# Kernel tuning notes

Measured on AMD Instinct MI355X. Metric: run time of the kernel, lower is better.

The kernel has to match this reference:

```python
import jax, jax.numpy as jnp
import numpy as np

B, S, D, H = 2, 2048, 1024, 16
DK = D // H


def setup_inputs() -> dict:
    key = jax.random.key(0)
    ks = jax.random.split(key, 8)
    q = jax.random.normal(ks[0], (B, S, D), dtype=jnp.float32)
    k = jax.random.normal(ks[1], (B, S, D), dtype=jnp.float32)
    v = jax.random.normal(ks[2], (B, S, D), dtype=jnp.float32)
    mask = jax.random.randint(ks[3], (B, 1, S, S), 0, 2, dtype=jnp.int32)
    sc = 1.0 / np.sqrt(D)
    Wq = jax.random.normal(ks[4], (D, D), dtype=jnp.float32) * sc
    Wk = jax.random.normal(ks[5], (D, D), dtype=jnp.float32) * sc
    Wv = jax.random.normal(ks[6], (D, D), dtype=jnp.float32) * sc
    Wo = jax.random.normal(ks[7], (D, D), dtype=jnp.float32) * sc
    return {"q": q, "k": k, "v": v, "mask": mask, "Wq": Wq, "Wk": Wk, "Wv": Wv, "Wo": Wo}


def reference(q, k, v, mask, Wq, Wk, Wv, Wo):
    # Linear projections (torch Linear: x @ W.T; bias=False). Weights here stored
    # as [D, D] applied as x @ W (equivalent parameterization).
    query = q @ Wq  # [B,S,D]
    key = k @ Wk
    value = v @ Wv
    # split heads -> [B,H,S,DK]
    query = query.reshape(B, S, H, DK).transpose(0, 2, 1, 3)
    key = key.reshape(B, S, H, DK).transpose(0, 2, 1, 3)
    value = value.reshape(B, S, H, DK).transpose(0, 2, 1, 3)
    scores = jnp.einsum('bhqd,bhkd->bhqk', query, key) / jnp.sqrt(jnp.float32(DK))
    scores = jnp.where(mask == 0, jnp.float32(-1e9), scores)
    probs = jax.nn.softmax(scores, axis=-1)  # dropout p=0.0 -> identity
    x = jnp.einsum('bhqk,bhkd->bhqd', probs, value)
    x = x.transpose(0, 2, 1, 3).reshape(B, S, D)
    return x @ Wo
```

## Files before the change

kernel.cpp:

```cpp
#include <hip/hip_runtime.h>
#include <hip/hip_bf16.h>
#include <math.h>

#define B_ 2
#define S_ 2048
#define D_ 1024
#define H_ 16
#define DK_ 64
#define SW_ (S_ / 64)

typedef unsigned short u16;
typedef unsigned int u32;
typedef unsigned long long u64;
typedef __attribute__((ext_vector_type(8))) short short8;
typedef __attribute__((ext_vector_type(4))) float float4_;
typedef __attribute__((ext_vector_type(4))) unsigned int uint4_;

static __device__ inline u16 f_to_bf16(float f) {
    union { float f; u32 i; } x; x.f = f;
    u32 r = x.i + 0x7fff + ((x.i >> 16) & 1);
    return (u16)(r >> 16);
}

static __device__ __forceinline__ u32 cvtpk(float a, float b) {
    u32 r;
    asm("v_cvt_pk_bf16_f32 %0, %1, %2" : "=v"(r) : "v"(a), "v"(b));
    return r;
}

static __device__ __forceinline__ float fast_exp2(float x) {
#if __has_builtin(__builtin_amdgcn_exp2f)
    return __builtin_amdgcn_exp2f(x);
#else
    return exp2f(x);
#endif
}

static __device__ inline void gl_lds16(const u16* g, u16* l) {
    __builtin_amdgcn_global_load_lds((const __attribute__((address_space(1))) void*)g,
                                     (__attribute__((address_space(3))) void*)l, 16, 0, 0);
}

__global__ __launch_bounds__(256) void prep(const float* __restrict__ q,
                                            const float* __restrict__ k,
                                            const float* __restrict__ v,
                                            const int* __restrict__ mask,
                                            const float* __restrict__ W0,
                                            const float* __restrict__ W1,
                                            const float* __restrict__ W2,
                                            const float* __restrict__ W3,
                                            u16* __restrict__ qb, u16* __restrict__ kb,
                                            u16* __restrict__ vb,
                                            u16* __restrict__ T0, u16* __restrict__ T1,
                                            u16* __restrict__ T2, u16* __restrict__ T3,
                                            u64* __restrict__ mpk) {
    __shared__ float tile[32][33];
    int gx = blockIdx.x, tid = threadIdx.x;
    if (gx < 6144) {
        int z = gx >> 11;
        int bx = gx & 2047;
        const float* s = (z == 0) ? q : ((z == 1) ? k : v);
        u16* d = (z == 0) ? qb : ((z == 1) ? kb : vb);
        int i = (bx * 256 + tid) * 8;
        #pragma unroll
        for (int j = 0; j < 8; ++j) d[i + j] = f_to_bf16(s[i + j]);
    } else if (gx < 10240) {
        int g2 = gx - 6144;
        int z = g2 >> 10;
        int rem = g2 & 1023;
        const float* W = (z == 0) ? W0 : ((z == 1) ? W1 : ((z == 2) ? W2 : W3));
        u16* Wt = (z == 0) ? T0 : ((z == 1) ? T1 : ((z == 2) ? T2 : T3));
        int k0 = (rem >> 5) * 32, n0 = (rem & 31) * 32;
        int tx = tid & 31, ty = tid >> 5;
        #pragma unroll
        for (int i2 = 0; i2 < 4; ++i2) {
            int row = ty + i2 * 8;
            tile[row][tx] = W[(size_t)(k0 + row) * D_ + n0 + tx];
        }
        __syncthreads();
        #pragma unroll
        for (int i2 = 0; i2 < 4; ++i2) {
            int row = ty + i2 * 8;
            Wt[(size_t)(n0 + row) * D_ + k0 + tx] = f_to_bf16(tile[tx][row]);
        }
    } else {
        int g3 = gx - 10240;
        int wv = (g3 * 256 + tid) >> 6;
        int lane = tid & 63;
        #pragma unroll
        for (int i2 = 0; i2 < 8; ++i2) {
            int wd = wv * 8 + i2;
            u64 bits = __ballot(mask[(size_t)wd * 64 + lane] != 0);
            if (lane == 0) mpk[wd] = bits;
        }
    }
}

static __device__ __forceinline__ void gemm128_body(u16* lds,
                                                    const u16* __restrict__ A,
                                                    const u16* __restrict__ Bt,
                                                    int K, float4_ (&acc)[4][4]) {
    u16* ldsA = lds;
    u16* ldsB = lds + 4096;
    int tm = blockIdx.x, tn = blockIdx.y;
    int t = threadIdx.x, l = t & 63;
    int w = t >> 6, wr = w >> 1, wc = w & 1;
    int colL = l & 15, grp = l >> 4;
    int sw4 = (grp ^ ((colL >> 1) & 3)) << 3;
    int f0 = t, f1 = t + 256;
    int row0 = f0 >> 2, kc0 = (((f0 & 3) ^ ((f0 >> 3) & 3)) << 3);
    int row1 = f1 >> 2, kc1 = (((f1 & 3) ^ ((f1 >> 3) & 3)) << 3);
    const u16* gA0 = A  + (size_t)(tm * 128 + row0) * K + kc0;
    const u16* gA1 = A  + (size_t)(tm * 128 + row1) * K + kc1;
    const u16* gB0 = Bt + (size_t)(tn * 128 + row0) * K + kc0;
    const u16* gB1 = Bt + (size_t)(tn * 128 + row1) * K + kc1;

    #pragma unroll
    for (int mi = 0; mi < 4; ++mi)
        #pragma unroll
        for (int ni = 0; ni < 4; ++ni)
            acc[mi][ni] = (float4_){0.f, 0.f, 0.f, 0.f};

    for (int k0 = 0; k0 < K; k0 += 32) {
        __syncthreads();
        gl_lds16(gA0 + k0, ldsA + f0 * 8);
        gl_lds16(gA1 + k0, ldsA + f1 * 8);
        gl_lds16(gB0 + k0, ldsB + f0 * 8);
        gl_lds16(gB1 + k0, ldsB + f1 * 8);
        __syncthreads();
        short8 a[4], b[4];
        #pragma unroll
        for (int mi = 0; mi < 4; ++mi)
            a[mi] = *(const short8*)&ldsA[(wr * 64 + mi * 16 + colL) * 32 + sw4];
        #pragma unroll
        for (int ni = 0; ni < 4; ++ni)
            b[ni] = *(const short8*)&ldsB[(wc * 64 + ni * 16 + colL) * 32 + sw4];
        #pragma unroll
        for (int mi = 0; mi < 4; ++mi)
            #pragma unroll
            for (int ni = 0; ni < 4; ++ni)
                acc[mi][ni] = __builtin_amdgcn_mfma_f32_16x16x32_bf16(a[mi], b[ni], acc[mi][ni], 0, 0, 0);
    }
}

__global__ __launch_bounds__(256, 3) void gemm_qkv(const u16* __restrict__ qb,
                                                   const u16* __restrict__ kb,
                                                   const u16* __restrict__ vb,
                                                   const u16* __restrict__ Wqt,
                                                   const u16* __restrict__ Wkt,
                                                   const u16* __restrict__ Wvt,
                                                   u16* __restrict__ Qp,
                                                   u16* __restrict__ Kp,
                                                   u16* __restrict__ Vt) {
    __shared__ u16 lds[8192];
    int z = blockIdx.z;
    const u16* A  = (z == 0) ? qb  : ((z == 1) ? kb  : vb);
    const u16* Bt = (z == 0) ? Wqt : ((z == 1) ? Wkt : Wvt);
    float4_ acc[4][4];
    gemm128_body(lds, A, Bt, D_, acc);

    int tm = blockIdx.x, tn = blockIdx.y;
    int t = threadIdx.x, l = t & 63;
    int w = t >> 6, wr = w >> 1, wc = w & 1;
    int colL = l & 15, grp = l >> 4;

    if (z < 2) {
        u16* Y = (z == 0) ? Qp : Kp;
        float sc = (z == 0) ? (0.125f * 1.44269504f) : 1.0f;
        #pragma unroll
        for (int mi = 0; mi < 4; ++mi)
            #pragma unroll
            for (int ni = 0; ni < 4; ++ni)
                #pragma unroll
                for (int r = 0; r < 4; ++r)
                    Y[(size_t)(tm * 128 + wr * 64 + mi * 16 + grp * 4 + r) * D_
                      + tn * 128 + wc * 64 + ni * 16 + colL] = f_to_bf16(acc[mi][ni][r] * sc);
    } else {
        int tok_base = tm * 128 + wr * 64;
        int bb = tok_base >> 11;
        int s_hi = tok_base & (S_ - 1);
        #pragma unroll
        for (int mi = 0; mi < 4; ++mi)
            #pragma unroll
            for (int ni = 0; ni < 4; ++ni) {
                int n  = tn * 128 + wc * 64 + ni * 16 + colL;
                int hh = n >> 6, dk = n & 63;
                u16* vp = Vt + ((size_t)(bb * H_ + hh) * DK_ + dk) * S_ + s_hi;
                #pragma unroll
                for (int r = 0; r < 4; ++r) {
                    int m = mi * 16 + grp * 4 + r;
                    int mp_ = ((m >> 5) & 1) * 32 + ((m >> 2) & 3) * 8 + ((m >> 4) & 1) * 4 + (m & 3);
                    vp[mp_] = f_to_bf16(acc[mi][ni][r]);
                }
            }
    }
}

__global__ __launch_bounds__(256, 3) void gemm_out(const u16* __restrict__ Xa,
                                                   const u16* __restrict__ Wot,
                                                   float* __restrict__ out) {
    __shared__ u16 lds[8192];
    float4_ acc[4][4];
    gemm128_body(lds, Xa, Wot, D_, acc);

    int tm = blockIdx.x, tn = blockIdx.y;
    int t = threadIdx.x, l = t & 63;
    int w = t >> 6, wr = w >> 1, wc = w & 1;
    int colL = l & 15, grp = l >> 4;
    #pragma unroll
    for (int mi = 0; mi < 4; ++mi)
        #pragma unroll
        for (int ni = 0; ni < 4; ++ni)
            #pragma unroll
            for (int r = 0; r < 4; ++r)
                out[(size_t)(tm * 128 + wr * 64 + mi * 16 + grp * 4 + r) * D_
                    + tn * 128 + wc * 64 + ni * 16 + colL] = acc[mi][ni][r];
}

__global__ __launch_bounds__(256, 2) void attn128(const u16* __restrict__ Qp,
                                                  const u16* __restrict__ Kp,
                                                  const u16* __restrict__ Vt,
                                                  const u64* __restrict__ mp,
                                                  u16* __restrict__ Xa) {
    __shared__ u16 ldsK[128 * 64];
    __shared__ u16 ldsV[2 * 64 * 64];

    int bid = blockIdx.x;
    int qt = bid & 15, h = (bid >> 4) & 15, b = bid >> 8;
    int t = threadIdx.x, l = t & 63, w = t >> 6;
    int colL = l & 15, grp = l >> 4;

    const u16* qbA = Qp + (size_t)(b * S_ + qt * 128 + w * 32 + colL) * D_ + h * DK_;
    const u16* qbB = qbA + (size_t)16 * D_;
    short8 qfA0 = *(const short8*)(qbA + grp * 8);
    short8 qfA1 = *(const short8*)(qbA + 32 + grp * 8);
    short8 qfB0 = *(const short8*)(qbB + grp * 8);
    short8 qfB1 = *(const short8*)(qbB + 32 + grp * 8);

    const u16* gK[4];
    const u16* gV[4];
    #pragma unroll
    for (int i = 0; i < 4; ++i) {
        int f = t + 256 * i;
        int krow = f >> 3, kch = (((f & 7) ^ (krow & 7)) << 3);
        gK[i] = Kp + (size_t)(b * S_ + krow) * D_ + h * DK_ + kch;
        int hreg = f >> 9, fp = f & 511;
        int vrow = fp >> 3, vch = (((fp & 7) ^ (vrow & 7)) << 3);
        gV[i] = Vt + ((size_t)(b * H_ + h) * DK_ + vrow) * S_ + hreg * 64 + vch;
    }

    int sw8 = (grp ^ (colL & 7)) << 3;

    short8 onesb;
    #pragma unroll
    for (int j = 0; j < 8; ++j) onesb[j] = (short)0x3F80;

    float4_ laccA = (float4_){0.f, 0.f, 0.f, 0.f};
    float4_ laccB = (float4_){0.f, 0.f, 0.f, 0.f};
    float4_ oA[4], oB[4];
    #pragma unroll
    for (int nt = 0; nt < 4; ++nt) {
        oA[nt] = (float4_){0.f, 0.f, 0.f, 0.f};
        oB[nt] = (float4_){0.f, 0.f, 0.f, 0.f};
    }

    const u64* mrA = mp + (size_t)(b * S_ + qt * 128 + w * 32 + colL) * SW_;
    const u64* mrB = mrA + (size_t)16 * SW_;

    for (int kt = 0; kt < S_; kt += 128) {
        u64 mwA0 = mrA[(kt >> 6)];
        u64 mwA1 = mrA[(kt >> 6) + 1];
        u64 mwB0 = mrB[(kt >> 6)];
        u64 mwB1 = mrB[(kt >> 6) + 1];

        __syncthreads();
        #pragma unroll
        for (int i = 0; i < 4; ++i) {
            int f = t + 256 * i;
            gl_lds16(gK[i] + (size_t)kt * D_, ldsK + f * 8);
            gl_lds16(gV[i] + kt,              ldsV + f * 8);
        }
        __syncthreads();

        float4_ sA[8], sB[8];
        __builtin_amdgcn_s_setprio(1);
        #pragma unroll
        for (int nt = 0; nt < 8; ++nt) {
            int ro = (nt * 16 + colL) * 64;
            short8 kf0 = *(const short8*)&ldsK[ro + sw8];
            short8 kf1 = *(const short8*)&ldsK[ro + (sw8 ^ 32)];
            sA[nt] = (float4_){0.f, 0.f, 0.f, 0.f};
            sA[nt] = __builtin_amdgcn_mfma_f32_16x16x32_bf16(kf0, qfA0, sA[nt], 0, 0, 0);
            sA[nt] = __builtin_amdgcn_mfma_f32_16x16x32_bf16(kf1, qfA1, sA[nt], 0, 0, 0);
            sB[nt] = (float4_){0.f, 0.f, 0.f, 0.f};
            sB[nt] = __builtin_amdgcn_mfma_f32_16x16x32_bf16(kf0, qfB0, sB[nt], 0, 0, 0);
            sB[nt] = __builtin_amdgcn_mfma_f32_16x16x32_bf16(kf1, qfB1, sB[nt], 0, 0, 0);
        }
        __builtin_amdgcn_s_setprio(0);

        u64 mshA0 = mwA0 >> (grp * 4), mshA1 = mwA1 >> (grp * 4);
        u64 mshB0 = mwB0 >> (grp * 4), mshB1 = mwB1 >> (grp * 4);
        #pragma unroll
        for (int nt = 0; nt < 8; ++nt) {
            u32 bitsA = ((u32)((nt < 4 ? mshA0 : mshA1) >> ((nt & 3) * 16))) & 15u;
            u32 bitsB = ((u32)((nt < 4 ? mshB0 : mshB1) >> ((nt & 3) * 16))) & 15u;
            #pragma unroll
            for (int r = 0; r < 4; ++r) {
                float pA = fast_exp2(sA[nt][r]);
                float pB = fast_exp2(sB[nt][r]);
                u32 keepA = 0u - ((bitsA >> r) & 1u);
                u32 keepB = 0u - ((bitsB >> r) & 1u);
                union { float f; u32 i; } ua, ub;
                ua.f = pA; ua.i &= keepA; sA[nt][r] = ua.f;
                ub.f = pB; ub.i &= keepB; sB[nt][r] = ub.f;
            }
        }

        short8 pfA[4], pfB[4];
        #pragma unroll
        for (int j = 0; j < 4; ++j) {
            uint4_ Ax = { cvtpk(sA[2 * j][0], sA[2 * j][1]), cvtpk(sA[2 * j][2], sA[2 * j][3]),
                          cvtpk(sA[2 * j + 1][0], sA[2 * j + 1][1]), cvtpk(sA[2 * j + 1][2], sA[2 * j + 1][3]) };
            pfA[j] = __builtin_bit_cast(short8, Ax);
            uint4_ Bx = { cvtpk(sB[2 * j][0], sB[2 * j][1]), cvtpk(sB[2 * j][2], sB[2 * j][3]),
                          cvtpk(sB[2 * j + 1][0], sB[2 * j + 1][1]), cvtpk(sB[2 * j + 1][2], sB[2 * j + 1][3]) };
            pfB[j] = __builtin_bit_cast(short8, Bx);
        }

        __builtin_amdgcn_s_setprio(1);
        #pragma unroll
        for (int nt = 0; nt < 4; ++nt) {
            int ro = (nt * 16 + colL) * 64;
            short8 vf0 = *(const short8*)&ldsV[ro + sw8];
            short8 vf1 = *(const short8*)&ldsV[ro + (sw8 ^ 32)];
            short8 vf2 = *(const short8*)&ldsV[4096 + ro + sw8];
            short8 vf3 = *(const short8*)&ldsV[4096 + ro + (sw8 ^ 32)];
            oA[nt] = __builtin_amdgcn_mfma_f32_16x16x32_bf16(pfA[0], vf0, oA[nt], 0, 0, 0);
            oA[nt] = __builtin_amdgcn_mfma_f32_16x16x32_bf16(pfA[1], vf1, oA[nt], 0, 0, 0);
            oA[nt] = __builtin_amdgcn_mfma_f32_16x16x32_bf16(pfA[2], vf2, oA[nt], 0, 0, 0);
            oA[nt] = __builtin_amdgcn_mfma_f32_16x16x32_bf16(pfA[3], vf3, oA[nt], 0, 0, 0);
            oB[nt] = __builtin_amdgcn_mfma_f32_16x16x32_bf16(pfB[0], vf0, oB[nt], 0, 0, 0);
            oB[nt] = __builtin_amdgcn_mfma_f32_16x16x32_bf16(pfB[1], vf1, oB[nt], 0, 0, 0);
            oB[nt] = __builtin_amdgcn_mfma_f32_16x16x32_bf16(pfB[2], vf2, oB[nt], 0, 0, 0);
            oB[nt] = __builtin_amdgcn_mfma_f32_16x16x32_bf16(pfB[3], vf3, oB[nt], 0, 0, 0);
        }
        laccA = __builtin_amdgcn_mfma_f32_16x16x32_bf16(pfA[0], onesb, laccA, 0, 0, 0);
        laccA = __builtin_amdgcn_mfma_f32_16x16x32_bf16(pfA[1], onesb, laccA, 0, 0, 0);
        laccA = __builtin_amdgcn_mfma_f32_16x16x32_bf16(pfA[2], onesb, laccA, 0, 0, 0);
        laccA = __builtin_amdgcn_mfma_f32_16x16x32_bf16(pfA[3], onesb, laccA, 0, 0, 0);
        laccB = __builtin_amdgcn_mfma_f32_16x16x32_bf16(pfB[0], onesb, laccB, 0, 0, 0);
        laccB = __builtin_amdgcn_mfma_f32_16x16x32_bf16(pfB[1], onesb, laccB, 0, 0, 0);
        laccB = __builtin_amdgcn_mfma_f32_16x16x32_bf16(pfB[2], onesb, laccB, 0, 0, 0);
        laccB = __builtin_amdgcn_mfma_f32_16x16x32_bf16(pfB[3], onesb, laccB, 0, 0, 0);
        __builtin_amdgcn_s_setprio(0);
    }

    float invA[4], invB[4];
    #pragma unroll
    for (int r = 0; r < 4; ++r) {
        invA[r] = 1.f / laccA[r];
        invB[r] = 1.f / laccB[r];
    }

    u16* xoA = Xa + (size_t)(b * S_ + qt * 128 + w * 32 + grp * 4) * D_ + h * DK_;
    u16* xoB = xoA + (size_t)16 * D_;
    #pragma unroll
    for (int r = 0; r < 4; ++r)
        #pragma unroll
        for (int nt = 0; nt < 4; ++nt) {
            xoA[(size_t)r * D_ + nt * 16 + colL] = f_to_bf16(oA[nt][r] * invA[r]);
            xoB[(size_t)r * D_ + nt * 16 + colL] = f_to_bf16(oB[nt][r] * invB[r]);
        }
}

extern "C" void kernel_launch(void* const* d_in, const int* in_sizes, int n_in,
                              void* d_out, int out_size, void* d_ws, size_t ws_size,
                              hipStream_t stream) {
    const float* q    = (const float*)d_in[0];
    const float* k    = (const float*)d_in[1];
    const float* v    = (const float*)d_in[2];
    const int*   mask = (const int*)d_in[3];
    const float* Wq   = (const float*)d_in[4];
    const float* Wk   = (const float*)d_in[5];
    const float* Wv   = (const float*)d_in[6];
    const float* Wo   = (const float*)d_in[7];
    float* out = (float*)d_out;

    const int NQ = B_ * S_ * D_;
    const int NW = D_ * D_;

    u16* qb  = (u16*)d_ws;
    u16* kb  = qb  + NQ;
    u16* vb  = kb  + NQ;
    u16* Wqt = vb  + NQ;
    u16* Wkt = Wqt + NW;
    u16* Wvt = Wkt + NW;
    u16* Wot = Wvt + NW;
    u16* Qp  = Wot + NW;
    u16* Kp  = Qp  + NQ;
    u16* Vt  = Kp  + NQ;
    u16* Xa  = Vt  + NQ;
    u64* mpk = (u64*)(Xa + NQ);

    dim3 cblk(256);
    prep<<<14336, cblk, 0, stream>>>(q, k, v, mask, Wq, Wk, Wv, Wo,
                                     qb, kb, vb, Wqt, Wkt, Wvt, Wot, mpk);

    const int M = B_ * S_;
    gemm_qkv<<<dim3(M / 128, D_ / 128, 3), cblk, 0, stream>>>(qb, kb, vb, Wqt, Wkt, Wvt, Qp, Kp, Vt);

    attn128<<<B_ * H_ * (S_ / 128), cblk, 0, stream>>>(Qp, Kp, Vt, mpk, Xa);

    gemm_out<<<dim3(M / 128, D_ / 128), cblk, 0, stream>>>(Xa, Wot, out);
}
```

Baseline: 242.4 us.

## Double-buffer K/V tiles in LDS to overlap loads with attention compute

The attention kernel now keeps two LDS buffers each for K and V. The first tile is preloaded, and the loads for the next 128-key tile are issued before computing on the current one, with a single barrier at the end of each iteration. This is meant to hide global-to-LDS load latency that the previous load-then-barrier-then-compute pattern exposed. LDS use per block doubles to 64KB, which could limit how many blocks fit on a CU. Correctness relies on the end-of-iteration barrier also waiting for the outstanding async loads.

```diff
diff --git a/kernel.cpp b/kernel.cpp
--- a/kernel.cpp
+++ b/kernel.cpp
@@ -222,8 +222,8 @@
                                                   const u16* __restrict__ Vt,
                                                   const u64* __restrict__ mp,
                                                   u16* __restrict__ Xa) {
-    __shared__ u16 ldsK[128 * 64];
-    __shared__ u16 ldsV[2 * 64 * 64];
+    __shared__ u16 ldsK[2 * 128 * 64];
+    __shared__ u16 ldsV[2 * 2 * 64 * 64];
 
     int bid = blockIdx.x;
     int qt = bid & 15, h = (bid >> 4) & 15, b = bid >> 8;
@@ -239,9 +239,11 @@
 
     const u16* gK[4];
     const u16* gV[4];
+    int fofs[4];
     #pragma unroll
     for (int i = 0; i < 4; ++i) {
         int f = t + 256 * i;
+        fofs[i] = f * 8;
         int krow = f >> 3, kch = (((f & 7) ^ (krow & 7)) << 3);
         gK[i] = Kp + (size_t)(b * S_ + krow) * D_ + h * DK_ + kch;
         int hreg = f >> 9, fp = f & 511;
@@ -267,28 +269,39 @@
     const u64* mrA = mp + (size_t)(b * S_ + qt * 128 + w * 32 + colL) * SW_;
     const u64* mrB = mrA + (size_t)16 * SW_;
 
+    #pragma unroll
+    for (int i = 0; i < 4; ++i) {
+        gl_lds16(gK[i], ldsK + fofs[i]);
+        gl_lds16(gV[i], ldsV + fofs[i]);
+    }
+    __syncthreads();
+
+    int cur = 0;
     for (int kt = 0; kt < S_; kt += 128) {
         u64 mwA0 = mrA[(kt >> 6)];
         u64 mwA1 = mrA[(kt >> 6) + 1];
         u64 mwB0 = mrB[(kt >> 6)];
         u64 mwB1 = mrB[(kt >> 6) + 1];
 
-        __syncthreads();
-        #pragma unroll
-        for (int i = 0; i < 4; ++i) {
-            int f = t + 256 * i;
-            gl_lds16(gK[i] + (size_t)kt * D_, ldsK + f * 8);
-            gl_lds16(gV[i] + kt,              ldsV + f * 8);
-        }
-        __syncthreads();
+        if (kt + 128 < S_) {
+            int nb = (cur ^ 1) * 8192;
+            #pragma unroll
+            for (int i = 0; i < 4; ++i) {
+                gl_lds16(gK[i] + (size_t)(kt + 128) * D_, ldsK + nb + fofs[i]);
+                gl_lds16(gV[i] + (kt + 128),              ldsV + nb + fofs[i]);
+            }
+        }
+
+        const u16* K_ = ldsK + cur * 8192;
+        const u16* V_ = ldsV + cur * 8192;
 
         float4_ sA[8], sB[8];
         __builtin_amdgcn_s_setprio(1);
         #pragma unroll
         for (int nt = 0; nt < 8; ++nt) {
             int ro = (nt * 16 + colL) * 64;
-            short8 kf0 = *(const short8*)&ldsK[ro + sw8];
-            short8 kf1 = *(const short8*)&ldsK[ro + (sw8 ^ 32)];
+            short8 kf0 = *(const short8*)&K_[ro + sw8];
+            short8 kf1 = *(const short8*)&K_[ro + (sw8 ^ 32)];
             sA[nt] = (float4_){0.f, 0.f, 0.f, 0.f};
             sA[nt] = __builtin_amdgcn_mfma_f32_16x16x32_bf16(kf0, qfA0, sA[nt], 0, 0, 0);
             sA[nt] = __builtin_amdgcn_mfma_f32_16x16x32_bf16(kf1, qfA1, sA[nt], 0, 0, 0);
@@ -331,10 +344,10 @@
         #pragma unroll
         for (int nt = 0; nt < 4; ++nt) {
             int ro = (nt * 16 + colL) * 64;
-            short8 vf0 = *(const short8*)&ldsV[ro + sw8];
-            short8 vf1 = *(const short8*)&ldsV[ro + (sw8 ^ 32)];
-            short8 vf2 = *(const short8*)&ldsV[4096 + ro + sw8];
-            short8 vf3 = *(const short8*)&ldsV[4096 + ro + (sw8 ^ 32)];
+            short8 vf0 = *(const short8*)&V_[ro + sw8];
+            short8 vf1 = *(const short8*)&V_[ro + (sw8 ^ 32)];
+            short8 vf2 = *(const short8*)&V_[4096 + ro + sw8];
+            short8 vf3 = *(const short8*)&V_[4096 + ro + (sw8 ^ 32)];
             oA[nt] = __builtin_amdgcn_mfma_f32_16x16x32_bf16(pfA[0], vf0, oA[nt], 0, 0, 0);
             oA[nt] = __builtin_amdgcn_mfma_f32_16x16x32_bf16(pfA[1], vf1, oA[nt], 0, 0, 0);
             oA[nt] = __builtin_amdgcn_mfma_f32_16x16x32_bf16(pfA[2], vf2, oA[nt], 0, 0, 0);
@@ -353,6 +366,9 @@
         laccB = __builtin_amdgcn_mfma_f32_16x16x32_bf16(pfB[2], onesb, laccB, 0, 0, 0);
         laccB = __builtin_amdgcn_mfma_f32_16x16x32_bf16(pfB[3], onesb, laccB, 0, 0, 0);
         __builtin_amdgcn_s_setprio(0);
+
+        __syncthreads();
+        cur ^= 1;
     }
 
     float invA[4], invB[4];
```

New measurement: 244.9 us. About the same (+1.1%).
